# Kernel optimization log

Measured on AMD Instinct MI355X. Metric: run time of the kernel, lower is better.

## Reference

```python
import jax, jax.numpy as jnp
import numpy as np

N = 100_000      # nodes
E = 1_600_000    # edges (before self loops)
IN = 128         # in_dim
HID = 64         # hidden_dim (per head)
HEADS = 2
NEG_SLOPE = 0.2  # PyG GATConv default negative_slope


def setup_inputs() -> dict:
    key = jax.random.key(0)
    k = jax.random.split(key, 6)
    x = jax.random.normal(k[0], (N, IN), jnp.float32)
    edge_index = jax.random.randint(k[1], (2, E), 0, N, dtype=jnp.int64)
    # GATConv linear (no bias in lin, bias added after aggregation in PyG)
    W = jax.random.normal(k[2], (IN, HEADS * HID), jnp.float32) * (1.0 / np.sqrt(IN))
    att_src = jax.random.normal(k[3], (HEADS, HID), jnp.float32) * 0.1
    att_dst = jax.random.normal(k[4], (HEADS, HID), jnp.float32) * 0.1
    bias = jnp.zeros((HEADS * HID,), jnp.float32)
    prelu_w = jnp.full((HEADS * HID,), 0.25, jnp.float32)  # nn.PReLU default init
    return {"x": x, "edge_index": edge_index, "W": W, "att_src": att_src,
            "att_dst": att_dst, "bias": bias, "prelu_w": prelu_w}


def reference(x, edge_index, W, att_src, att_dst, bias, prelu_w):
    n = x.shape[0]
    h = (x @ W).reshape(n, HEADS, HID)                 # [N,H,C]
    a_s = jnp.einsum('nhc,hc->nh', h, att_src)         # [N,H]
    a_d = jnp.einsum('nhc,hc->nh', h, att_dst)         # [N,H]
    # add self loops (PyG default add_self_loops=True)
    loops = jnp.arange(n, dtype=edge_index.dtype)
    src = jnp.concatenate([edge_index[0], loops])      # [Et]
    dst = jnp.concatenate([edge_index[1], loops])      # [Et]
    logits = a_s[src] + a_d[dst]                       # [Et,H]
    logits = jnp.where(logits >= 0, logits, NEG_SLOPE * logits)  # LeakyReLU
    # segment softmax over destination neighborhoods
    m = jax.ops.segment_max(logits, dst, num_segments=n)         # [N,H]
    e = jnp.exp(logits - m[dst])
    s = jax.ops.segment_sum(e, dst, num_segments=n)              # [N,H]
    alpha = e / (s[dst] + 1e-16)                                 # [Et,H]
    # (attention dropout p=0.2 is identity in eval mode)
    msg = h[src] * alpha[..., None]                    # [Et,H,C]
    out = jax.ops.segment_sum(msg, dst, num_segments=n).reshape(n, HEADS * HID)
    out = out + bias
    # PReLU with per-channel weight
    return jnp.where(out >= 0, out, prelu_w * out)
```

## Files before the change

kernel.cpp:

```cpp
#include <hip/hip_runtime.h>
#include <hip/hip_fp16.h>
#include <hip/hip_bf16.h>
#include <cstdint>
#include <cstddef>

#define NEG_SLOPE 0.2f
#define BSH 8
#define BNODES 256
#define CAP 5120
#define SLOTS 48

typedef __attribute__((ext_vector_type(8))) short short8v;
typedef __attribute__((ext_vector_type(4))) float f32x4;
typedef __attribute__((ext_vector_type(2))) uint32_t u32x2;

__device__ __forceinline__ uint32_t bf16pair(float a, float b) {
    __hip_bfloat162 h = __float22bfloat162_rn(make_float2(a, b));
    return *reinterpret_cast<uint32_t*>(&h);
}
__device__ __forceinline__ uint16_t rne16(float f) {
    uint32_t u = __float_as_uint(f);
    return (uint16_t)((u + 0x7fffu + ((u >> 16) & 1u)) >> 16);
}
__device__ __forceinline__ float bflo(uint32_t u) { return __uint_as_float(u << 16); }
__device__ __forceinline__ float bfhi(uint32_t u) { return __uint_as_float(u & 0xffff0000u); }
__device__ __forceinline__ uint32_t packf16(float a, float b) {
    __half2 h = __floats2half2_rn(a, b);
    return *reinterpret_cast<uint32_t*>(&h);
}

__global__ __launch_bounds__(256, 3) void gemm_scatter(
    const float* __restrict__ x, const float* __restrict__ W,
    const float* __restrict__ att_src, const float* __restrict__ att_dst,
    uint32_t* __restrict__ hb, float* __restrict__ a_s, float* __restrict__ a_d,
    const int* __restrict__ src, const int* __restrict__ dst,
    int* __restrict__ gcur, uint32_t* __restrict__ pairs,
    int e, int nb, int n, int nbs)
{
    constexpr int PW = 136;
    __shared__ __align__(16) char smem[52224];
    const int tid = threadIdx.x;

    if (blockIdx.x < nbs) {
        int* histL  = (int*)smem;
        int* gbaseL = histL + 512;
        const int t0 = blockIdx.x * 4096;

        for (int i = tid; i < nb; i += 256) histL[i] = 0;
        __syncthreads();

        int      myb[16];
        int      myslot[16];
        uint32_t mypk[16];
#pragma unroll 16
        for (int k = 0; k < 16; ++k) {
            int i = t0 + tid + k * 256;
            if (i < e) {
                int s = __builtin_nontemporal_load(src + i);
                int d = __builtin_nontemporal_load(dst + i);
                int b = d >> BSH;
                myb[k]    = b;
                mypk[k]   = (uint32_t)s | ((uint32_t)(d & (BNODES - 1)) << 17);
                myslot[k] = atomicAdd(&histL[b], 1);
            } else myb[k] = -1;
        }
        __syncthreads();
        for (int i = tid; i < nb; i += 256) {
            int c = histL[i];
            gbaseL[i] = c ? atomicAdd(&gcur[i], c) : 0;
        }
        __syncthreads();
#pragma unroll 16
        for (int k = 0; k < 16; ++k) {
            if (myb[k] >= 0) {
                int p = gbaseL[myb[k]] + myslot[k];
                if (p < CAP) pairs[(size_t)myb[k] * CAP + p] = mypk[k];
            }
        }
        return;
    }

    unsigned short* Wt = (unsigned short*)smem;
    unsigned short* Hs = (unsigned short*)(smem + 34816);
    const int w    = tid >> 6;
    const int lane = tid & 63;
    const int cl   = lane & 15;
    const int gq   = lane >> 4;
    const int base = (blockIdx.x - nbs) * 64;

    const float4* W4 = (const float4*)W;
#pragma unroll
    for (int i = 0; i < 8; ++i) {
        int idx = tid + i * 256;
        int k   = (idx >> 5) * 2, c4 = (idx & 31) * 4;
        float4 v0 = W4[k * 32 + (idx & 31)];
        float4 v1 = W4[(k + 1) * 32 + (idx & 31)];
        *(uint32_t*)&Wt[(c4 + 0) * PW + k] = bf16pair(v0.x, v1.x);
        *(uint32_t*)&Wt[(c4 + 1) * PW + k] = bf16pair(v0.y, v1.y);
        *(uint32_t*)&Wt[(c4 + 2) * PW + k] = bf16pair(v0.z, v1.z);
        *(uint32_t*)&Wt[(c4 + 3) * PW + k] = bf16pair(v0.w, v1.w);
    }

    float asr[8], adr[8];
#pragma unroll
    for (int t = 0; t < 8; ++t) {
        asr[t] = att_src[t * 16 + cl];
        adr[t] = att_dst[t * 16 + cl];
    }
    __syncthreads();

    const int rowg = base + w * 16 + cl;
    const int rowc = rowg < n ? rowg : (n - 1);
    const f32x4* xp = (const f32x4*)(x + (size_t)rowc * 128);

    f32x4 acc[8];
#pragma unroll
    for (int t = 0; t < 8; ++t) acc[t] = (f32x4){0.f, 0.f, 0.f, 0.f};

#pragma unroll
    for (int s = 0; s < 4; ++s) {
        int kq = s * 8 + gq * 2;
        f32x4 f0 = __builtin_nontemporal_load(xp + kq);
        f32x4 f1 = __builtin_nontemporal_load(xp + kq + 1);
        union { short8v v; uint32_t d[4]; } A;
        A.d[0] = bf16pair(f0.x, f0.y);
        A.d[1] = bf16pair(f0.z, f0.w);
        A.d[2] = bf16pair(f1.x, f1.y);
        A.d[3] = bf16pair(f1.z, f1.w);
#pragma unroll
        for (int t = 0; t < 8; ++t) {
            union { short8v v; uint4 q; } B;
            B.q = *(const uint4*)&Wt[(t * 16 + cl) * PW + s * 32 + gq * 8];
            acc[t] = __builtin_amdgcn_mfma_f32_16x16x32_bf16(A.v, B.v, acc[t], 0, 0, 0);
        }
    }

    float ps0[4], ps1[4], pd0[4], pd1[4];
#pragma unroll
    for (int r = 0; r < 4; ++r) { ps0[r] = ps1[r] = pd0[r] = pd1[r] = 0.f; }
#pragma unroll
    for (int t = 0; t < 8; ++t) {
#pragma unroll
        for (int r = 0; r < 4; ++r) {
            float v = acc[t][r];
            if (t < 4) { ps0[r] = fmaf(v, asr[t], ps0[r]); pd0[r] = fmaf(v, adr[t], pd0[r]); }
            else       { ps1[r] = fmaf(v, asr[t], ps1[r]); pd1[r] = fmaf(v, adr[t], pd1[r]); }
        }
    }
#pragma unroll
    for (int off = 1; off < 16; off <<= 1) {
#pragma unroll
        for (int r = 0; r < 4; ++r) {
            ps0[r] += __shfl_xor(ps0[r], off);
            ps1[r] += __shfl_xor(ps1[r], off);
            pd0[r] += __shfl_xor(pd0[r], off);
            pd1[r] += __shfl_xor(pd1[r], off);
        }
    }
    if (cl == 0) {
#pragma unroll
        for (int r = 0; r < 4; ++r) {
            int rg = base + w * 16 + gq * 4 + r;
            if (rg < n) {
                a_s[rg * 2 + 0] = ps0[r]; a_s[rg * 2 + 1] = ps1[r];
                a_d[rg * 2 + 0] = pd0[r]; a_d[rg * 2 + 1] = pd1[r];
            }
        }
    }

#pragma unroll
    for (int t = 0; t < 8; ++t) {
#pragma unroll
        for (int r = 0; r < 4; ++r) {
            int row = gq * 4 + r;
            Hs[(size_t)w * 16 * PW + row * PW + t * 16 + cl] = rne16(acc[t][r]);
        }
    }
    __syncthreads();
#pragma unroll
    for (int q = 0; q < 4; ++q) {
        int row = q * 4 + gq;
        int cu  = 4 * cl;
        uint4 v = *(const uint4*)&Hs[(size_t)w * 16 * PW + row * PW + cu * 2];
        int rg = base + w * 16 + row;
        if (rg < n) *(uint4*)&hb[(size_t)rg * 64 + cu] = v;
    }
}

#define KMAX (CAP / 512)
__global__ __launch_bounds__(512) void build_csr(
    const uint32_t* __restrict__ pairs, const int* __restrict__ gcur,
    const float* __restrict__ a_s, const float* __restrict__ a_d,
    uint32_t* __restrict__ meta, uint2* __restrict__ edges, int n, int nb)
{
    __shared__ int curL[BNODES];
    __shared__ float adL[BNODES * 2];
    const int b = blockIdx.x, tid = threadIdx.x;
    const int nbase = b * BNODES;
    const int nodes = min(BNODES, n - nbase);
    const int C = min(gcur[b], CAP);

    if (tid < BNODES) curL[tid] = 1;
    float es0 = 0.f, es1 = 0.f;
    if (tid < nodes) {
        int g = nbase + tid;
        float2 ad = ((const float2*)a_d)[g];
        adL[2 * tid]     = ad.x;
        adL[2 * tid + 1] = ad.y;
        float2 as = ((const float2*)a_s)[g];
        float l0 = as.x + ad.x; l0 = l0 >= 0.f ? l0 : NEG_SLOPE * l0;
        float l1 = as.y + ad.y; l1 = l1 >= 0.f ? l1 : NEG_SLOPE * l1;
        es0 = __expf(l0); es1 = __expf(l1);
    }
    __syncthreads();

    uint32_t pk[KMAX];
    float2   asv[KMAX];
#pragma unroll
    for (int k = 0; k < KMAX; ++k) {
        int i = tid + k * 512;
        if (i < C) pk[k] = __builtin_nontemporal_load(pairs + (size_t)b * CAP + i);
    }
#pragma unroll
    for (int k = 0; k < KMAX; ++k) {
        int i = tid + k * 512;
        if (i < C) asv[k] = ((const float2*)a_s)[pk[k] & 0x1FFFF];
    }
    if (tid < nodes)
        edges[(size_t)(nbase + tid) * SLOTS] =
            make_uint2((uint32_t)(nbase + tid), packf16(es0, es1));

#pragma unroll
    for (int k = 0; k < KMAX; ++k) {
        int i = tid + k * 512;
        if (i < C) {
            int dl = pk[k] >> 17;
            int s  = pk[k] & 0x1FFFF;
            float l0 = asv[k].x + adL[2 * dl];     l0 = l0 >= 0.f ? l0 : NEG_SLOPE * l0;
            float l1 = asv[k].y + adL[2 * dl + 1]; l1 = l1 >= 0.f ? l1 : NEG_SLOPE * l1;
            float e0 = __expf(l0), e1 = __expf(l1);
            int slot = atomicAdd(&curL[dl], 1);
            if (slot < SLOTS)
                edges[(size_t)(nbase + dl) * SLOTS + slot] =
                    make_uint2((uint32_t)s, packf16(e0, e1));
        }
    }
    __syncthreads();
    if (tid < nodes) meta[nbase + tid] = (uint32_t)min(curL[tid], SLOTS);
}

__global__ __launch_bounds__(256, 8) void attn_agg(
    const uint32_t* __restrict__ hb, const uint2* __restrict__ edges,
    const uint32_t* __restrict__ meta,
    const float* __restrict__ bias, const float* __restrict__ prelu_w,
    float* __restrict__ out, int n)
{
    const int wv   = (blockIdx.x * blockDim.x + threadIdx.x) >> 6;
    const int lane = threadIdx.x & 63;
    const int gwA  = wv * 2;
    if (gwA >= n) return;
    const int h = lane >> 5, hlane = lane & 31;
    const int gw = gwA + h;
    const bool act = gw < n;
    const int deg = act ? (int)meta[gw] : 0;
    const size_t start = (size_t)gw * SLOTS;
    const uint4* hb4 = (const uint4*)hb;

    if (__all(deg <= 32)) {
        int sv = 0; float e0 = 0.f, e1 = 0.f;
        if (hlane < deg) {
            u32x2 ed = __builtin_nontemporal_load((const u32x2*)(edges + start + hlane));
            sv = (int)ed.x;
            uint32_t ey = ed.y;
            __half2 h2 = *reinterpret_cast<__half2*>(&ey);
            e0 = __half2float(__low2half(h2));
            e1 = __half2float(__high2half(h2));
        }
        float s0 = e0, s1 = e1;
#pragma unroll
        for (int off = 16; off > 0; off >>= 1) {
            s0 += __shfl_xor(s0, off);
            s1 += __shfl_xor(s1, off);
        }
        const float inv0 = 1.f / (s0 + 1e-16f);
        const float inv1 = 1.f / (s1 + 1e-16f);

        const int g = (lane >> 4) & 1, r = lane & 15;
        const int sbase = h * 32;
        float acc[8];
#pragma unroll
        for (int q = 0; q < 8; ++q) acc[q] = 0.f;

        const int iters = (deg + 7) >> 3;
        for (int jj = 0; jj < iters; ++jj) {
            const int j0 = jj * 8 + g * 4;
            int   s0v = __shfl(sv, sbase + j0);
            int   s1v = __shfl(sv, sbase + j0 + 1);
            int   s2v = __shfl(sv, sbase + j0 + 2);
            int   s3v = __shfl(sv, sbase + j0 + 3);
            float A00 = __shfl(e0, sbase + j0),     A10 = __shfl(e1, sbase + j0);
            float A01 = __shfl(e0, sbase + j0 + 1), A11 = __shfl(e1, sbase + j0 + 1);
            float A02 = __shfl(e0, sbase + j0 + 2), A12 = __shfl(e1, sbase + j0 + 2);
            float A03 = __shfl(e0, sbase + j0 + 3), A13 = __shfl(e1, sbase + j0 + 3);
            float Aa = (r < 8) ? A00 : A10;
            float Ab = (r < 8) ? A01 : A11;
            float Ac = (r < 8) ? A02 : A12;
            float Ad = (r < 8) ? A03 : A13;
            uint4 qa = hb4[(size_t)s0v * 16 + r];
            uint4 qb = hb4[(size_t)s1v * 16 + r];
            uint4 qc = hb4[(size_t)s2v * 16 + r];
            uint4 qd = hb4[(size_t)s3v * 16 + r];
            acc[0] = fmaf(Aa, bflo(qa.x), acc[0]); acc[1] = fmaf(Aa, bfhi(qa.x), acc[1]);
            acc[2] = fmaf(Aa, bflo(qa.y), acc[2]); acc[3] = fmaf(Aa, bfhi(qa.y), acc[3]);
            acc[4] = fmaf(Aa, bflo(qa.z), acc[4]); acc[5] = fmaf(Aa, bfhi(qa.z), acc[5]);
            acc[6] = fmaf(Aa, bflo(qa.w), acc[6]); acc[7] = fmaf(Aa, bfhi(qa.w), acc[7]);
            acc[0] = fmaf(Ab, bflo(qb.x), acc[0]); acc[1] = fmaf(Ab, bfhi(qb.x), acc[1]);
            acc[2] = fmaf(Ab, bflo(qb.y), acc[2]); acc[3] = fmaf(Ab, bfhi(qb.y), acc[3]);
            acc[4] = fmaf(Ab, bflo(qb.z), acc[4]); acc[5] = fmaf(Ab, bfhi(qb.z), acc[5]);
            acc[6] = fmaf(Ab, bflo(qb.w), acc[6]); acc[7] = fmaf(Ab, bfhi(qb.w), acc[7]);
            acc[0] = fmaf(Ac, bflo(qc.x), acc[0]); acc[1] = fmaf(Ac, bfhi(qc.x), acc[1]);
            acc[2] = fmaf(Ac, bflo(qc.y), acc[2]); acc[3] = fmaf(Ac, bfhi(qc.y), acc[3]);
            acc[4] = fmaf(Ac, bflo(qc.z), acc[4]); acc[5] = fmaf(Ac, bfhi(qc.z), acc[5]);
            acc[6] = fmaf(Ac, bflo(qc.w), acc[6]); acc[7] = fmaf(Ac, bfhi(qc.w), acc[7]);
            acc[0] = fmaf(Ad, bflo(qd.x), acc[0]); acc[1] = fmaf(Ad, bfhi(qd.x), acc[1]);
            acc[2] = fmaf(Ad, bflo(qd.y), acc[2]); acc[3] = fmaf(Ad, bfhi(qd.y), acc[3]);
            acc[4] = fmaf(Ad, bflo(qd.z), acc[4]); acc[5] = fmaf(Ad, bfhi(qd.z), acc[5]);
            acc[6] = fmaf(Ad, bflo(qd.w), acc[6]); acc[7] = fmaf(Ad, bfhi(qd.w), acc[7]);
        }
#pragma unroll
        for (int q = 0; q < 8; ++q) acc[q] += __shfl_xor(acc[q], 16);

        if (hlane < 16 && act) {
            const float winv = (r < 8) ? inv0 : inv1;
            float4 b0 = ((const float4*)bias)[r * 2];
            float4 b1 = ((const float4*)bias)[r * 2 + 1];
            float4 p0 = ((const float4*)prelu_w)[r * 2];
            float4 p1 = ((const float4*)prelu_w)[r * 2 + 1];
            f32x4 w0, w1;
            w0.x = fmaf(acc[0], winv, b0.x); w0.x = w0.x >= 0.f ? w0.x : p0.x * w0.x;
            w0.y = fmaf(acc[1], winv, b0.y); w0.y = w0.y >= 0.f ? w0.y : p0.y * w0.y;
            w0.z = fmaf(acc[2], winv, b0.z); w0.z = w0.z >= 0.f ? w0.z : p0.z * w0.z;
            w0.w = fmaf(acc[3], winv, b0.w); w0.w = w0.w >= 0.f ? w0.w : p0.w * w0.w;
            w1.x = fmaf(acc[4], winv, b1.x); w1.x = w1.x >= 0.f ? w1.x : p1.x * w1.x;
            w1.y = fmaf(acc[5], winv, b1.y); w1.y = w1.y >= 0.f ? w1.y : p1.y * w1.y;
            w1.z = fmaf(acc[6], winv, b1.z); w1.z = w1.z >= 0.f ? w1.z : p1.z * w1.z;
            w1.w = fmaf(acc[7], winv, b1.w); w1.w = w1.w >= 0.f ? w1.w : p1.w * w1.w;
            float* op = out + (size_t)gw * 128 + r * 8;
            __builtin_nontemporal_store(w0, (f32x4*)op);
            __builtin_nontemporal_store(w1, (f32x4*)(op + 4));
        }
        return;
    }

    for (int pick = 0; pick < 2; ++pick) {
        const int gwp = gwA + pick;
        if (gwp >= n) continue;
        const int dg = (int)meta[gwp];
        const size_t st = (size_t)gwp * SLOTS;

        {
            int sv = 0; float e0 = 0.f, e1 = 0.f;
            if (lane < dg) {
                uint2 ed = edges[st + lane];
                sv = (int)ed.x;
                __half2 h2 = *reinterpret_cast<__half2*>(&ed.y);
                e0 = __half2float(__low2half(h2));
                e1 = __half2float(__high2half(h2));
            }
            float s0 = e0, s1 = e1;
#pragma unroll
            for (int off = 32; off > 0; off >>= 1) {
                s0 += __shfl_xor(s0, off);
                s1 += __shfl_xor(s1, off);
            }
            const float inv0 = 1.f / (s0 + 1e-16f);
            const float inv1 = 1.f / (s1 + 1e-16f);
            const int g = lane >> 4, r = lane & 15;
            float acc[8];
#pragma unroll
            for (int q = 0; q < 8; ++q) acc[q] = 0.f;
            const int iters = (dg + 15) >> 4;
            for (int jj = 0; jj < iters; ++jj) {
                const int j0 = jj * 16 + g;
                int   s0v = __shfl(sv, j0);
                int   s1v = __shfl(sv, j0 + 4);
                int   s2v = __shfl(sv, j0 + 8);
                int   s3v = __shfl(sv, j0 + 12);
                float A00 = __shfl(e0, j0),      A10 = __shfl(e1, j0);
                float A01 = __shfl(e0, j0 + 4),  A11 = __shfl(e1, j0 + 4);
                float A02 = __shfl(e0, j0 + 8),  A12 = __shfl(e1, j0 + 8);
                float A03 = __shfl(e0, j0 + 12), A13 = __shfl(e1, j0 + 12);
                float Aa = (r < 8) ? A00 : A10;
                float Ab = (r < 8) ? A01 : A11;
                float Ac = (r < 8) ? A02 : A12;
                float Ad = (r < 8) ? A03 : A13;
                uint4 qa = hb4[(size_t)s0v * 16 + r];
                uint4 qb = hb4[(size_t)s1v * 16 + r];
                uint4 qc = hb4[(size_t)s2v * 16 + r];
                uint4 qd = hb4[(size_t)s3v * 16 + r];
                acc[0] = fmaf(Aa, bflo(qa.x), acc[0]); acc[1] = fmaf(Aa, bfhi(qa.x), acc[1]);
                acc[2] = fmaf(Aa, bflo(qa.y), acc[2]); acc[3] = fmaf(Aa, bfhi(qa.y), acc[3]);
                acc[4] = fmaf(Aa, bflo(qa.z), acc[4]); acc[5] = fmaf(Aa, bfhi(qa.z), acc[5]);
                acc[6] = fmaf(Aa, bflo(qa.w), acc[6]); acc[7] = fmaf(Aa, bfhi(qa.w), acc[7]);
                acc[0] = fmaf(Ab, bflo(qb.x), acc[0]); acc[1] = fmaf(Ab, bfhi(qb.x), acc[1]);
                acc[2] = fmaf(Ab, bflo(qb.y), acc[2]); acc[3] = fmaf(Ab, bfhi(qb.y), acc[3]);
                acc[4] = fmaf(Ab, bflo(qb.z), acc[4]); acc[5] = fmaf(Ab, bfhi(qb.z), acc[5]);
                acc[6] = fmaf(Ab, bflo(qb.w), acc[6]); acc[7] = fmaf(Ab, bfhi(qb.w), acc[7]);
                acc[0] = fmaf(Ac, bflo(qc.x), acc[0]); acc[1] = fmaf(Ac, bfhi(qc.x), acc[1]);
                acc[2] = fmaf(Ac, bflo(qc.y), acc[2]); acc[3] = fmaf(Ac, bfhi(qc.y), acc[3]);
                acc[4] = fmaf(Ac, bflo(qc.z), acc[4]); acc[5] = fmaf(Ac, bfhi(qc.z), acc[5]);
                acc[6] = fmaf(Ac, bflo(qc.w), acc[6]); acc[7] = fmaf(Ac, bfhi(qc.w), acc[7]);
                acc[0] = fmaf(Ad, bflo(qd.x), acc[0]); acc[1] = fmaf(Ad, bfhi(qd.x), acc[1]);
                acc[2] = fmaf(Ad, bflo(qd.y), acc[2]); acc[3] = fmaf(Ad, bfhi(qd.y), acc[3]);
                acc[4] = fmaf(Ad, bflo(qd.z), acc[4]); acc[5] = fmaf(Ad, bfhi(qd.z), acc[5]);
                acc[6] = fmaf(Ad, bflo(qd.w), acc[6]); acc[7] = fmaf(Ad, bfhi(qd.w), acc[7]);
            }
#pragma unroll
            for (int q = 0; q < 8; ++q) {
                acc[q] += __shfl_xor(acc[q], 16);
                acc[q] += __shfl_xor(acc[q], 32);
            }
            if (lane < 16) {
                const float winv = (lane < 8) ? inv0 : inv1;
                float4 b0 = ((const float4*)bias)[lane * 2];
                float4 b1 = ((const float4*)bias)[lane * 2 + 1];
                float4 p0 = ((const float4*)prelu_w)[lane * 2];
                float4 p1 = ((const float4*)prelu_w)[lane * 2 + 1];
                f32x4 w0, w1;
                w0.x = fmaf(acc[0], winv, b0.x); w0.x = w0.x >= 0.f ? w0.x : p0.x * w0.x;
                w0.y = fmaf(acc[1], winv, b0.y); w0.y = w0.y >= 0.f ? w0.y : p0.y * w0.y;
                w0.z = fmaf(acc[2], winv, b0.z); w0.z = w0.z >= 0.f ? w0.z : p0.z * w0.z;
                w0.w = fmaf(acc[3], winv, b0.w); w0.w = w0.w >= 0.f ? w0.w : p0.w * w0.w;
                w1.x = fmaf(acc[4], winv, b1.x); w1.x = w1.x >= 0.f ? w1.x : p1.x * w1.x;
                w1.y = fmaf(acc[5], winv, b1.y); w1.y = w1.y >= 0.f ? w1.y : p1.y * w1.y;
                w1.z = fmaf(acc[6], winv, b1.z); w1.z = w1.z >= 0.f ? w1.z : p1.z * w1.z;
                w1.w = fmaf(acc[7], winv, b1.w); w1.w = w1.w >= 0.f ? w1.w : p1.w * w1.w;
                float* op = out + (size_t)gwp * 128 + lane * 8;
                __builtin_nontemporal_store(w0, (f32x4*)op);
                __builtin_nontemporal_store(w1, (f32x4*)(op + 4));
            }
        }
    }
}

extern "C" void kernel_launch(void* const* d_in, const int* in_sizes, int n_in,
                              void* d_out, int out_size, void* d_ws, size_t ws_size,
                              hipStream_t stream)
{
    const float* x        = (const float*)d_in[0];
    const int*   ei       = (const int*)d_in[1];
    const float* W        = (const float*)d_in[2];
    const float* att_src  = (const float*)d_in[3];
    const float* att_dst  = (const float*)d_in[4];
    const float* bias     = (const float*)d_in[5];
    const float* prelu_w  = (const float*)d_in[6];
    float* out = (float*)d_out;

    const int n = in_sizes[0] / 128;
    const int e = in_sizes[1] / 2;
    const int* srcp = ei;
    const int* dstp = ei + e;
    const int nb  = (n + BNODES - 1) / BNODES;
    const int nbs = (e + 4095) / 4096;
    const int nbg = (n + 63) / 64;

    uint32_t* hb    = (uint32_t*)d_ws;
    uint32_t* meta  = (uint32_t*)(hb + (size_t)n * 64);
    float*    a_s   = (float*)(meta + n);
    float*    a_d   = a_s + (size_t)n * 2;
    int*      gcur  = (int*)(a_d + (size_t)n * 2);
    uint32_t* pairs = (uint32_t*)(gcur + 512);
    uint2*    edges = (uint2*)(pairs + (size_t)nb * CAP);

    hipMemsetAsync(gcur, 0, 512 * sizeof(int), stream);
    gemm_scatter<<<nbs + nbg, 256, 0, stream>>>(x, W, att_src, att_dst,
                                                hb, a_s, a_d, srcp, dstp,
                                                gcur, pairs, e, nb, n, nbs);
    build_csr<<<nb, 512, 0, stream>>>(pairs, gcur, a_s, a_d, meta, edges, n, nb);
    const int nwv = (n + 1) / 2;
    attn_agg<<<(nwv + 3) / 4, 256, 0, stream>>>(hb, edges, meta, bias, prelu_w, out, n);
}
```

Before: 139.1 us.

## Move edge logit/exp computation from CSR build into aggregation kernel

The CSR build kernel now writes only source column indices (4 bytes per edge) instead of index plus packed fp16 exp weights, and no longer gathers a_s or computes exponentials. The aggregation kernel gathers a_s for each neighbor and a_d for the destination and computes the LeakyReLU and exp itself. This halves the edge-list write and read traffic and shortens build_csr, at the cost of an extra random a_s gather in the latency-bound aggregation loop. Attention weights are also now kept in fp32 rather than rounded to fp16.

```diff
diff --git a/kernel.cpp b/kernel.cpp
--- a/kernel.cpp
+++ b/kernel.cpp
@@ -12,7 +12,6 @@
 
 typedef __attribute__((ext_vector_type(8))) short short8v;
 typedef __attribute__((ext_vector_type(4))) float f32x4;
-typedef __attribute__((ext_vector_type(2))) uint32_t u32x2;
 
 __device__ __forceinline__ uint32_t bf16pair(float a, float b) {
     __hip_bfloat162 h = __float22bfloat162_rn(make_float2(a, b));
@@ -24,10 +23,6 @@
 }
 __device__ __forceinline__ float bflo(uint32_t u) { return __uint_as_float(u << 16); }
 __device__ __forceinline__ float bfhi(uint32_t u) { return __uint_as_float(u & 0xffff0000u); }
-__device__ __forceinline__ uint32_t packf16(float a, float b) {
-    __half2 h = __floats2half2_rn(a, b);
-    return *reinterpret_cast<uint32_t*>(&h);
-}
 
 __global__ __launch_bounds__(256, 3) void gemm_scatter(
     const float* __restrict__ x, const float* __restrict__ W,
@@ -187,71 +182,37 @@
     }
 }
 
-#define KMAX (CAP / 512)
-__global__ __launch_bounds__(512) void build_csr(
+__global__ __launch_bounds__(512) void build_cols(
     const uint32_t* __restrict__ pairs, const int* __restrict__ gcur,
-    const float* __restrict__ a_s, const float* __restrict__ a_d,
-    uint32_t* __restrict__ meta, uint2* __restrict__ edges, int n, int nb)
+    uint32_t* __restrict__ meta, uint32_t* __restrict__ cols, int n, int nb)
 {
     __shared__ int curL[BNODES];
-    __shared__ float adL[BNODES * 2];
     const int b = blockIdx.x, tid = threadIdx.x;
     const int nbase = b * BNODES;
     const int nodes = min(BNODES, n - nbase);
     const int C = min(gcur[b], CAP);
 
     if (tid < BNODES) curL[tid] = 1;
-    float es0 = 0.f, es1 = 0.f;
-    if (tid < nodes) {
-        int g = nbase + tid;
-        float2 ad = ((const float2*)a_d)[g];
-        adL[2 * tid]     = ad.x;
-        adL[2 * tid + 1] = ad.y;
-        float2 as = ((const float2*)a_s)[g];
-        float l0 = as.x + ad.x; l0 = l0 >= 0.f ? l0 : NEG_SLOPE * l0;
-        float l1 = as.y + ad.y; l1 = l1 >= 0.f ? l1 : NEG_SLOPE * l1;
-        es0 = __expf(l0); es1 = __expf(l1);
-    }
     __syncthreads();
-
-    uint32_t pk[KMAX];
-    float2   asv[KMAX];
-#pragma unroll
-    for (int k = 0; k < KMAX; ++k) {
-        int i = tid + k * 512;
-        if (i < C) pk[k] = __builtin_nontemporal_load(pairs + (size_t)b * CAP + i);
-    }
-#pragma unroll
-    for (int k = 0; k < KMAX; ++k) {
-        int i = tid + k * 512;
-        if (i < C) asv[k] = ((const float2*)a_s)[pk[k] & 0x1FFFF];
-    }
     if (tid < nodes)
-        edges[(size_t)(nbase + tid) * SLOTS] =
-            make_uint2((uint32_t)(nbase + tid), packf16(es0, es1));
-
-#pragma unroll
-    for (int k = 0; k < KMAX; ++k) {
-        int i = tid + k * 512;
-        if (i < C) {
-            int dl = pk[k] >> 17;
-            int s  = pk[k] & 0x1FFFF;
-            float l0 = asv[k].x + adL[2 * dl];     l0 = l0 >= 0.f ? l0 : NEG_SLOPE * l0;
-            float l1 = asv[k].y + adL[2 * dl + 1]; l1 = l1 >= 0.f ? l1 : NEG_SLOPE * l1;
-            float e0 = __expf(l0), e1 = __expf(l1);
-            int slot = atomicAdd(&curL[dl], 1);
-            if (slot < SLOTS)
-                edges[(size_t)(nbase + dl) * SLOTS + slot] =
-                    make_uint2((uint32_t)s, packf16(e0, e1));
-        }
+        cols[(size_t)(nbase + tid) * SLOTS] = (uint32_t)(nbase + tid);
+
+    for (int i = tid; i < C; i += 512) {
+        uint32_t p = __builtin_nontemporal_load(pairs + (size_t)b * CAP + i);
+        int dl = p >> 17;
+        int s  = p & 0x1FFFF;
+        int slot = atomicAdd(&curL[dl], 1);
+        if (slot < SLOTS)
+            cols[(size_t)(nbase + dl) * SLOTS + slot] = (uint32_t)s;
     }
     __syncthreads();
     if (tid < nodes) meta[nbase + tid] = (uint32_t)min(curL[tid], SLOTS);
 }
 
 __global__ __launch_bounds__(256, 8) void attn_agg(
-    const uint32_t* __restrict__ hb, const uint2* __restrict__ edges,
+    const uint32_t* __restrict__ hb, const uint32_t* __restrict__ cols,
     const uint32_t* __restrict__ meta,
+    const float* __restrict__ a_s, const float* __restrict__ a_d,
     const float* __restrict__ bias, const float* __restrict__ prelu_w,
     float* __restrict__ out, int n)
 {
@@ -267,14 +228,15 @@
     const uint4* hb4 = (const uint4*)hb;
 
     if (__all(deg <= 32)) {
+        float2 ad = make_float2(0.f, 0.f);
+        if (act) ad = ((const float2*)a_d)[gw];
         int sv = 0; float e0 = 0.f, e1 = 0.f;
         if (hlane < deg) {
-            u32x2 ed = __builtin_nontemporal_load((const u32x2*)(edges + start + hlane));
-            sv = (int)ed.x;
-            uint32_t ey = ed.y;
-            __half2 h2 = *reinterpret_cast<__half2*>(&ey);
-            e0 = __half2float(__low2half(h2));
-            e1 = __half2float(__high2half(h2));
+            sv = (int)__builtin_nontemporal_load(cols + start + hlane);
+            float2 as = ((const float2*)a_s)[sv];
+            float l0 = as.x + ad.x; l0 = l0 >= 0.f ? l0 : NEG_SLOPE * l0;
+            float l1 = as.y + ad.y; l1 = l1 >= 0.f ? l1 : NEG_SLOPE * l1;
+            e0 = __expf(l0); e1 = __expf(l1);
         }
         float s0 = e0, s1 = e1;
 #pragma unroll
@@ -357,88 +319,87 @@
         if (gwp >= n) continue;
         const int dg = (int)meta[gwp];
         const size_t st = (size_t)gwp * SLOTS;
-
-        {
-            int sv = 0; float e0 = 0.f, e1 = 0.f;
-            if (lane < dg) {
-                uint2 ed = edges[st + lane];
-                sv = (int)ed.x;
-                __half2 h2 = *reinterpret_cast<__half2*>(&ed.y);
-                e0 = __half2float(__low2half(h2));
-                e1 = __half2float(__high2half(h2));
-            }
-            float s0 = e0, s1 = e1;
-#pragma unroll
-            for (int off = 32; off > 0; off >>= 1) {
-                s0 += __shfl_xor(s0, off);
-                s1 += __shfl_xor(s1, off);
-            }
-            const float inv0 = 1.f / (s0 + 1e-16f);
-            const float inv1 = 1.f / (s1 + 1e-16f);
-            const int g = lane >> 4, r = lane & 15;
-            float acc[8];
-#pragma unroll
-            for (int q = 0; q < 8; ++q) acc[q] = 0.f;
-            const int iters = (dg + 15) >> 4;
-            for (int jj = 0; jj < iters; ++jj) {
-                const int j0 = jj * 16 + g;
-                int   s0v = __shfl(sv, j0);
-                int   s1v = __shfl(sv, j0 + 4);
-                int   s2v = __shfl(sv, j0 + 8);
-                int   s3v = __shfl(sv, j0 + 12);
-                float A00 = __shfl(e0, j0),      A10 = __shfl(e1, j0);
-                float A01 = __shfl(e0, j0 + 4),  A11 = __shfl(e1, j0 + 4);
-                float A02 = __shfl(e0, j0 + 8),  A12 = __shfl(e1, j0 + 8);
-                float A03 = __shfl(e0, j0 + 12), A13 = __shfl(e1, j0 + 12);
-                float Aa = (r < 8) ? A00 : A10;
-                float Ab = (r < 8) ? A01 : A11;
-                float Ac = (r < 8) ? A02 : A12;
-                float Ad = (r < 8) ? A03 : A13;
-                uint4 qa = hb4[(size_t)s0v * 16 + r];
-                uint4 qb = hb4[(size_t)s1v * 16 + r];
-                uint4 qc = hb4[(size_t)s2v * 16 + r];
-                uint4 qd = hb4[(size_t)s3v * 16 + r];
-                acc[0] = fmaf(Aa, bflo(qa.x), acc[0]); acc[1] = fmaf(Aa, bfhi(qa.x), acc[1]);
-                acc[2] = fmaf(Aa, bflo(qa.y), acc[2]); acc[3] = fmaf(Aa, bfhi(qa.y), acc[3]);
-                acc[4] = fmaf(Aa, bflo(qa.z), acc[4]); acc[5] = fmaf(Aa, bfhi(qa.z), acc[5]);
-                acc[6] = fmaf(Aa, bflo(qa.w), acc[6]); acc[7] = fmaf(Aa, bfhi(qa.w), acc[7]);
-                acc[0] = fmaf(Ab, bflo(qb.x), acc[0]); acc[1] = fmaf(Ab, bfhi(qb.x), acc[1]);
-                acc[2] = fmaf(Ab, bflo(qb.y), acc[2]); acc[3] = fmaf(Ab, bfhi(qb.y), acc[3]);
-                acc[4] = fmaf(Ab, bflo(qb.z), acc[4]); acc[5] = fmaf(Ab, bfhi(qb.z), acc[5]);
-                acc[6] = fmaf(Ab, bflo(qb.w), acc[6]); acc[7] = fmaf(Ab, bfhi(qb.w), acc[7]);
-                acc[0] = fmaf(Ac, bflo(qc.x), acc[0]); acc[1] = fmaf(Ac, bfhi(qc.x), acc[1]);
-                acc[2] = fmaf(Ac, bflo(qc.y), acc[2]); acc[3] = fmaf(Ac, bfhi(qc.y), acc[3]);
-                acc[4] = fmaf(Ac, bflo(qc.z), acc[4]); acc[5] = fmaf(Ac, bfhi(qc.z), acc[5]);
-                acc[6] = fmaf(Ac, bflo(qc.w), acc[6]); acc[7] = fmaf(Ac, bfhi(qc.w), acc[7]);
-                acc[0] = fmaf(Ad, bflo(qd.x), acc[0]); acc[1] = fmaf(Ad, bfhi(qd.x), acc[1]);
-                acc[2] = fmaf(Ad, bflo(qd.y), acc[2]); acc[3] = fmaf(Ad, bfhi(qd.y), acc[3]);
-                acc[4] = fmaf(Ad, bflo(qd.z), acc[4]); acc[5] = fmaf(Ad, bfhi(qd.z), acc[5]);
-                acc[6] = fmaf(Ad, bflo(qd.w), acc[6]); acc[7] = fmaf(Ad, bfhi(qd.w), acc[7]);
-            }
-#pragma unroll
-            for (int q = 0; q < 8; ++q) {
-                acc[q] += __shfl_xor(acc[q], 16);
-                acc[q] += __shfl_xor(acc[q], 32);
-            }
-            if (lane < 16) {
-                const float winv = (lane < 8) ? inv0 : inv1;
-                float4 b0 = ((const float4*)bias)[lane * 2];
-                float4 b1 = ((const float4*)bias)[lane * 2 + 1];
-                float4 p0 = ((const float4*)prelu_w)[lane * 2];
-                float4 p1 = ((const float4*)prelu_w)[lane * 2 + 1];
-                f32x4 w0, w1;
-                w0.x = fmaf(acc[0], winv, b0.x); w0.x = w0.x >= 0.f ? w0.x : p0.x * w0.x;
-                w0.y = fmaf(acc[1], winv, b0.y); w0.y = w0.y >= 0.f ? w0.y : p0.y * w0.y;
-                w0.z = fmaf(acc[2], winv, b0.z); w0.z = w0.z >= 0.f ? w0.z : p0.z * w0.z;
-                w0.w = fmaf(acc[3], winv, b0.w); w0.w = w0.w >= 0.f ? w0.w : p0.w * w0.w;
-                w1.x = fmaf(acc[4], winv, b1.x); w1.x = w1.x >= 0.f ? w1.x : p1.x * w1.x;
-                w1.y = fmaf(acc[5], winv, b1.y); w1.y = w1.y >= 0.f ? w1.y : p1.y * w1.y;
-                w1.z = fmaf(acc[6], winv, b1.z); w1.z = w1.z >= 0.f ? w1.z : p1.z * w1.z;
-                w1.w = fmaf(acc[7], winv, b1.w); w1.w = w1.w >= 0.f ? w1.w : p1.w * w1.w;
-                float* op = out + (size_t)gwp * 128 + lane * 8;
-                __builtin_nontemporal_store(w0, (f32x4*)op);
-                __builtin_nontemporal_store(w1, (f32x4*)(op + 4));
-            }
+        const float2 ad = ((const float2*)a_d)[gwp];
+
+        int sv = 0; float e0 = 0.f, e1 = 0.f;
+        if (lane < dg) {
+            sv = (int)cols[st + lane];
+            float2 as = ((const float2*)a_s)[sv];
+            float l0 = as.x + ad.x; l0 = l0 >= 0.f ? l0 : NEG_SLOPE * l0;
+            float l1 = as.y + ad.y; l1 = l1 >= 0.f ? l1 : NEG_SLOPE * l1;
+            e0 = __expf(l0); e1 = __expf(l1);
+        }
+        float s0 = e0, s1 = e1;
+#pragma unroll
+        for (int off = 32; off > 0; off >>= 1) {
+            s0 += __shfl_xor(s0, off);
+            s1 += __shfl_xor(s1, off);
+        }
+        const float inv0 = 1.f / (s0 + 1e-16f);
+        const float inv1 = 1.f / (s1 + 1e-16f);
+        const int g = lane >> 4, r = lane & 15;
+        float acc[8];
+#pragma unroll
+        for (int q = 0; q < 8; ++q) acc[q] = 0.f;
+        const int iters = (dg + 15) >> 4;
+        for (int jj = 0; jj < iters; ++jj) {
+            const int j0 = jj * 16 + g;
+            int   s0v = __shfl(sv, j0);
+            int   s1v = __shfl(sv, j0 + 4);
+            int   s2v = __shfl(sv, j0 + 8);
+            int   s3v = __shfl(sv, j0 + 12);
+            float A00 = __shfl(e0, j0),      A10 = __shfl(e1, j0);
+            float A01 = __shfl(e0, j0 + 4),  A11 = __shfl(e1, j0 + 4);
+            float A02 = __shfl(e0, j0 + 8),  A12 = __shfl(e1, j0 + 8);
+            float A03 = __shfl(e0, j0 + 12), A13 = __shfl(e1, j0 + 12);
+            float Aa = (r < 8) ? A00 : A10;
+            float Ab = (r < 8) ? A01 : A11;
+            float Ac = (r < 8) ? A02 : A12;
+            float Ad = (r < 8) ? A03 : A13;
+            uint4 qa = hb4[(size_t)s0v * 16 + r];
+            uint4 qb = hb4[(size_t)s1v * 16 + r];
+            uint4 qc = hb4[(size_t)s2v * 16 + r];
+            uint4 qd = hb4[(size_t)s3v * 16 + r];
+            acc[0] = fmaf(Aa, bflo(qa.x), acc[0]); acc[1] = fmaf(Aa, bfhi(qa.x), acc[1]);
+            acc[2] = fmaf(Aa, bflo(qa.y), acc[2]); acc[3] = fmaf(Aa, bfhi(qa.y), acc[3]);
+            acc[4] = fmaf(Aa, bflo(qa.z), acc[4]); acc[5] = fmaf(Aa, bfhi(qa.z), acc[5]);
+            acc[6] = fmaf(Aa, bflo(qa.w), acc[6]); acc[7] = fmaf(Aa, bfhi(qa.w), acc[7]);
+            acc[0] = fmaf(Ab, bflo(qb.x), acc[0]); acc[1] = fmaf(Ab, bfhi(qb.x), acc[1]);
+            acc[2] = fmaf(Ab, bflo(qb.y), acc[2]); acc[3] = fmaf(Ab, bfhi(qb.y), acc[3]);
+            acc[4] = fmaf(Ab, bflo(qb.z), acc[4]); acc[5] = fmaf(Ab, bfhi(qb.z), acc[5]);
+            acc[6] = fmaf(Ab, bflo(qb.w), acc[6]); acc[7] = fmaf(Ab, bfhi(qb.w), acc[7]);
+            acc[0] = fmaf(Ac, bflo(qc.x), acc[0]); acc[1] = fmaf(Ac, bfhi(qc.x), acc[1]);
+            acc[2] = fmaf(Ac, bflo(qc.y), acc[2]); acc[3] = fmaf(Ac, bfhi(qc.y), acc[3]);
+            acc[4] = fmaf(Ac, bflo(qc.z), acc[4]); acc[5] = fmaf(Ac, bfhi(qc.z), acc[5]);
+            acc[6] = fmaf(Ac, bflo(qc.w), acc[6]); acc[7] = fmaf(Ac, bfhi(qc.w), acc[7]);
+            acc[0] = fmaf(Ad, bflo(qd.x), acc[0]); acc[1] = fmaf(Ad, bfhi(qd.x), acc[1]);
+            acc[2] = fmaf(Ad, bflo(qd.y), acc[2]); acc[3] = fmaf(Ad, bfhi(qd.y), acc[3]);
+            acc[4] = fmaf(Ad, bflo(qd.z), acc[4]); acc[5] = fmaf(Ad, bfhi(qd.z), acc[5]);
+            acc[6] = fmaf(Ad, bflo(qd.w), acc[6]); acc[7] = fmaf(Ad, bfhi(qd.w), acc[7]);
+        }
+#pragma unroll
+        for (int q = 0; q < 8; ++q) {
+            acc[q] += __shfl_xor(acc[q], 16);
+            acc[q] += __shfl_xor(acc[q], 32);
+        }
+        if (lane < 16) {
+            const float winv = (lane < 8) ? inv0 : inv1;
+            float4 b0 = ((const float4*)bias)[lane * 2];
+            float4 b1 = ((const float4*)bias)[lane * 2 + 1];
+            float4 p0 = ((const float4*)prelu_w)[lane * 2];
+            float4 p1 = ((const float4*)prelu_w)[lane * 2 + 1];
+            f32x4 w0, w1;
+            w0.x = fmaf(acc[0], winv, b0.x); w0.x = w0.x >= 0.f ? w0.x : p0.x * w0.x;
+            w0.y = fmaf(acc[1], winv, b0.y); w0.y = w0.y >= 0.f ? w0.y : p0.y * w0.y;
+            w0.z = fmaf(acc[2], winv, b0.z); w0.z = w0.z >= 0.f ? w0.z : p0.z * w0.z;
+            w0.w = fmaf(acc[3], winv, b0.w); w0.w = w0.w >= 0.f ? w0.w : p0.w * w0.w;
+            w1.x = fmaf(acc[4], winv, b1.x); w1.x = w1.x >= 0.f ? w1.x : p1.x * w1.x;
+            w1.y = fmaf(acc[5], winv, b1.y); w1.y = w1.y >= 0.f ? w1.y : p1.y * w1.y;
+            w1.z = fmaf(acc[6], winv, b1.z); w1.z = w1.z >= 0.f ? w1.z : p1.z * w1.z;
+            w1.w = fmaf(acc[7], winv, b1.w); w1.w = w1.w >= 0.f ? w1.w : p1.w * w1.w;
+            float* op = out + (size_t)gwp * 128 + lane * 8;
+            __builtin_nontemporal_store(w0, (f32x4*)op);
+            __builtin_nontemporal_store(w1, (f32x4*)(op + 4));
         }
     }
 }
@@ -470,13 +431,14 @@
     float*    a_d   = a_s + (size_t)n * 2;
     int*      gcur  = (int*)(a_d + (size_t)n * 2);
     uint32_t* pairs = (uint32_t*)(gcur + 512);
-    uint2*    edges = (uint2*)(pairs + (size_t)nb * CAP);
+    uint32_t* cols  = (uint32_t*)(pairs + (size_t)nb * CAP);
 
     hipMemsetAsync(gcur, 0, 512 * sizeof(int), stream);
     gemm_scatter<<<nbs + nbg, 256, 0, stream>>>(x, W, att_src, att_dst,
                                                 hb, a_s, a_d, srcp, dstp,
                                                 gcur, pairs, e, nb, n, nbs);
-    build_csr<<<nb, 512, 0, stream>>>(pairs, gcur, a_s, a_d, meta, edges, n, nb);
+    build_cols<<<nb, 512, 0, stream>>>(pairs, gcur, meta, cols, n, nb);
     const int nwv = (n + 1) / 2;
-    attn_agg<<<(nwv + 3) / 4, 256, 0, stream>>>(hb, edges, meta, bias, prelu_w, out, n);
-}
+    attn_agg<<<(nwv + 3) / 4, 256, 0, stream>>>(hb, cols, meta, a_s, a_d,
+                                                bias, prelu_w, out, n);
+}
```

Measured after the change: 139.9 us. Within noise of the previous version (+0.6%).
